# Kernel tuning notes

Measured on AMD Instinct MI355X. Metric: run time of the kernel, lower is better.

The kernel has to match this reference:

```python
import jax, jax.numpy as jnp
import numpy as np

B, S, D = 8, 4096, 512
L = 8921  # n_labels (ICD9 full)

def setup_inputs() -> dict:
    key = jax.random.key(0)
    kx, ku = jax.random.split(key)
    x = jax.random.normal(kx, (B, S, D), dtype=jnp.float32)
    # xavier_uniform init for U [L, D]
    bound = jnp.sqrt(6.0 / (L + D)).astype(jnp.float32)
    U = jax.random.uniform(ku, (L, D), dtype=jnp.float32, minval=-bound, maxval=bound)
    return {"x": x, "U": U}

def reference(x, U):
    # scores: [B, L, S] = U @ x^T (unscaled)
    scores = jnp.einsum('ld,bsd->bls', U, x)
    alpha = jax.nn.softmax(scores, axis=2)  # softmax over sequence dim
    out = jnp.einsum('bls,bsd->bld', alpha, x)  # [B, L, D]
    return (out, alpha)
```

## Files before the change

### kernel.cpp

```cpp
#include <hip/hip_runtime.h>
#include <stdint.h>
#include <stddef.h>

#define BB 8
#define SS 4096
#define DD 512
#define LL 8921

typedef __attribute__((ext_vector_type(8))) short bf16x8;
typedef __attribute__((ext_vector_type(4))) float f32x4;
typedef __attribute__((ext_vector_type(4))) unsigned short u16x4;
typedef __attribute__((ext_vector_type(8))) unsigned short u16x8;

__device__ __forceinline__ unsigned short f2bf(float f) {
  union { float f; uint32_t u; } v; v.f = f;
  uint32_t r = (v.u + 0x7FFFu + ((v.u >> 16) & 1u)) >> 16;
  return (unsigned short)r;
}

__device__ __forceinline__ float bf2f(unsigned short h) {
  union { uint32_t u; float f; } v; v.u = ((uint32_t)h) << 16;
  return v.f;
}

__device__ __forceinline__ void gload_lds16(const void* g, void* l) {
  __builtin_amdgcn_global_load_lds(
      (__attribute__((address_space(1))) void*)(void*)g,
      (__attribute__((address_space(3))) void*)l, 16, 0, 0);
}

__device__ __forceinline__ f32x4 mfma16(bf16x8 a, bf16x8 b, f32x4 c) {
  return __builtin_amdgcn_mfma_f32_16x16x32_bf16(a, b, c, 0, 0, 0);
}

__global__ __launch_bounds__(256) void k_cvtU(const float* __restrict__ U,
                                              unsigned short* __restrict__ Ub) {
  const int idx = blockIdx.x * 256 + threadIdx.x;
  const int nchunk = (LL * DD) / 8;
  if (idx >= nchunk) return;
  const float4* s = (const float4*)U + (size_t)idx * 2;
  const float4 a = s[0], b = s[1];
  u16x8 h;
  h[0] = f2bf(a.x); h[1] = f2bf(a.y); h[2] = f2bf(a.z); h[3] = f2bf(a.w);
  h[4] = f2bf(b.x); h[5] = f2bf(b.y); h[6] = f2bf(b.z); h[7] = f2bf(b.w);
  *(u16x8*)(Ub + (size_t)idx * 8) = h;
}

__global__ __launch_bounds__(256) void k_cvtx(const float* __restrict__ x,
                                              unsigned short* __restrict__ xb,
                                              unsigned short* __restrict__ xT) {
  __shared__ unsigned short t[64][72];
  const int b = blockIdx.z;
  const int s0 = blockIdx.x * 64;
  const int d0 = blockIdx.y * 64;
  const int tid = threadIdx.x;
  const int rr = tid >> 4;
  const int cv = tid & 15;
#pragma unroll
  for (int i = 0; i < 4; ++i) {
    const int srow = rr + i * 16;
    const size_t gi = ((size_t)b * SS + s0 + srow) * DD + d0 + cv * 4;
    const float4 v = *(const float4*)&x[gi];
    u16x4 h;
    h[0] = f2bf(v.x); h[1] = f2bf(v.y); h[2] = f2bf(v.z); h[3] = f2bf(v.w);
    *(u16x4*)&xb[gi] = h;
    t[srow][cv * 4 + 0] = h[0]; t[srow][cv * 4 + 1] = h[1];
    t[srow][cv * 4 + 2] = h[2]; t[srow][cv * 4 + 3] = h[3];
  }
  __syncthreads();
#pragma unroll
  for (int i = 0; i < 4; ++i) {
    const int drow = rr + i * 16;
    u16x4 h;
    h[0] = t[cv * 4 + 0][drow]; h[1] = t[cv * 4 + 1][drow];
    h[2] = t[cv * 4 + 2][drow]; h[3] = t[cv * 4 + 3][drow];
    *(u16x4*)&xT[((size_t)b * DD + d0 + drow) * SS + s0 + cv * 4] = h;
  }
}


__global__ __launch_bounds__(256) void k_score2(const unsigned short* __restrict__ Ub,
                                                const unsigned short* __restrict__ xb,
                                                unsigned short* __restrict__ es,
                                                float* __restrict__ Z) {
  __shared__ unsigned short smem[2][128][64];
  const int tid = threadIdx.x;
  const int lane = tid & 63, wid = tid >> 6;
  const int wr = wid >> 1, wc = wid & 1;
  const int b = blockIdx.y;
  const int lt = blockIdx.x >> 5, st = blockIdx.x & 31;
  const int l0 = lt * 128, s0 = st * 128;
  const int fr = lane & 15, fq = lane >> 4;

  f32x4 acc[4][4];
#pragma unroll
  for (int m = 0; m < 4; ++m)
#pragma unroll
    for (int n = 0; n < 4; ++n) acc[m][n] = (f32x4){0.f, 0.f, 0.f, 0.f};

  for (int k0 = 0; k0 < DD; k0 += 64) {
#pragma unroll
    for (int r = 0; r < 4; ++r) {
      const int c = r * 256 + tid;
      const int row = c >> 3, col = (c & 7) * 8;
      int lrow = l0 + row; if (lrow > LL - 1) lrow = LL - 1;
      gload_lds16(Ub + (size_t)lrow * DD + k0 + col, (unsigned short*)smem[0] + c * 8);
      gload_lds16(xb + ((size_t)b * SS + s0 + row) * DD + k0 + col,
                  (unsigned short*)smem[1] + c * 8);
    }
    __syncthreads();
#pragma unroll
    for (int kk = 0; kk < 64; kk += 32) {
      bf16x8 af[4], bfv[4];
#pragma unroll
      for (int m = 0; m < 4; ++m)
        af[m] = *(const bf16x8*)&smem[0][wr * 64 + m * 16 + fr][kk + fq * 8];
#pragma unroll
      for (int n = 0; n < 4; ++n)
        bfv[n] = *(const bf16x8*)&smem[1][wc * 64 + n * 16 + fr][kk + fq * 8];
#pragma unroll
      for (int m = 0; m < 4; ++m)
#pragma unroll
        for (int n = 0; n < 4; ++n)
          acc[m][n] = mfma16(af[m], bfv[n], acc[m][n]);
    }
    __syncthreads();
  }

  float ev[4][4][4];
  float rsum[4][4];
#pragma unroll
  for (int m = 0; m < 4; ++m)
#pragma unroll
    for (int j = 0; j < 4; ++j) rsum[m][j] = 0.f;
#pragma unroll
  for (int m = 0; m < 4; ++m)
#pragma unroll
    for (int n = 0; n < 4; ++n)
#pragma unroll
      for (int j = 0; j < 4; ++j) {
        const float e = __expf(acc[m][n][j]);
        ev[m][n][j] = e;
        rsum[m][j] += e;
      }
#pragma unroll
  for (int m = 0; m < 4; ++m)
#pragma unroll
    for (int j = 0; j < 4; ++j) {
      float v = rsum[m][j];
      v += __shfl_xor(v, 1);
      v += __shfl_xor(v, 2);
      v += __shfl_xor(v, 4);
      v += __shfl_xor(v, 8);
      const int l = l0 + wr * 64 + m * 16 + fq * 4 + j;
      if (fr == 0 && l < LL) atomicAdd(&Z[b * LL + l], v);
    }
  unsigned short (*Es)[128] = (unsigned short (*)[128])smem;
#pragma unroll
  for (int m = 0; m < 4; ++m) {
    const int lr = wr * 64 + m * 16 + fq * 4;
#pragma unroll
    for (int n = 0; n < 4; ++n) {
      const int sc = wc * 64 + n * 16 + fr;
#pragma unroll
      for (int j = 0; j < 4; ++j) {
        const int ll = lr + j;
        Es[ll][sc ^ ((ll & 7) << 3)] = f2bf(ev[m][n][j]);
      }
    }
  }
  __syncthreads();
  {
    const int lr = tid >> 1;
    const int ch = (tid & 1) * 64;
    const int l = l0 + lr;
    if (l < LL) {
      unsigned short* dst = es + ((size_t)b * LL + l) * SS + s0 + ch;
#pragma unroll
      for (int w = 0; w < 8; ++w) {
        u16x8 hv = *(const u16x8*)&Es[lr][(ch + w * 8) ^ ((lr & 7) << 3)];
        *(u16x8*)(dst + w * 8) = hv;
      }
    }
  }
}

__global__ __launch_bounds__(256) void k_norm(const unsigned short* __restrict__ es,
                                              const float* __restrict__ Z,
                                              float* __restrict__ alpha) {
  const int row = blockIdx.x;
  const float rZ = 1.0f / Z[row];
  const unsigned short* src = es + (size_t)row * SS;
  float* dst = alpha + (size_t)row * SS;
  const int t = threadIdx.x;
#pragma unroll
  for (int i = 0; i < 2; ++i) {
    u16x8 h = *(const u16x8*)(src + t * 16 + i * 8);
    float4 a, b;
    a.x = bf2f(h[0]) * rZ; a.y = bf2f(h[1]) * rZ;
    a.z = bf2f(h[2]) * rZ; a.w = bf2f(h[3]) * rZ;
    b.x = bf2f(h[4]) * rZ; b.y = bf2f(h[5]) * rZ;
    b.z = bf2f(h[6]) * rZ; b.w = bf2f(h[7]) * rZ;
    *(float4*)(dst + t * 16 + i * 8) = a;
    *(float4*)(dst + t * 16 + i * 8 + 4) = b;
  }
}

__global__ __launch_bounds__(256) void k_pv2(const unsigned short* __restrict__ es,
                                             const unsigned short* __restrict__ xTb,
                                             const float* __restrict__ Z,
                                             float* __restrict__ out) {
  __shared__ unsigned short As[128][64];
  __shared__ unsigned short Bs[128][64];
  const int tid = threadIdx.x;
  const int lane = tid & 63, wid = tid >> 6;
  const int wr = wid >> 1, wc = wid & 1;
  const int b = blockIdx.y;
  const int lt = blockIdx.x >> 2, dt = blockIdx.x & 3;
  const int l0 = lt * 128, d0 = dt * 128;
  const int fr = lane & 15, fq = lane >> 4;

  f32x4 acc[4][4];
#pragma unroll
  for (int m = 0; m < 4; ++m)
#pragma unroll
    for (int n = 0; n < 4; ++n) acc[m][n] = (f32x4){0.f, 0.f, 0.f, 0.f};

  for (int k0 = 0; k0 < SS; k0 += 64) {
#pragma unroll
    for (int r = 0; r < 4; ++r) {
      const int c = r * 256 + tid;
      const int row = c >> 3, col = (c & 7) * 8;
      int lrow = l0 + row; if (lrow > LL - 1) lrow = LL - 1;
      gload_lds16(es + ((size_t)b * LL + lrow) * SS + k0 + col,
                  (unsigned short*)As + c * 8);
      gload_lds16(xTb + ((size_t)b * DD + d0 + row) * SS + k0 + col,
                  (unsigned short*)Bs + c * 8);
    }
    __syncthreads();
#pragma unroll
    for (int kk = 0; kk < 64; kk += 32) {
      bf16x8 af[4], bfv[4];
#pragma unroll
      for (int m = 0; m < 4; ++m)
        af[m] = *(const bf16x8*)&As[wr * 64 + m * 16 + fr][kk + fq * 8];
#pragma unroll
      for (int n = 0; n < 4; ++n)
        bfv[n] = *(const bf16x8*)&Bs[wc * 64 + n * 16 + fr][kk + fq * 8];
#pragma unroll
      for (int m = 0; m < 4; ++m)
#pragma unroll
        for (int n = 0; n < 4; ++n)
          acc[m][n] = mfma16(af[m], bfv[n], acc[m][n]);
    }
    __syncthreads();
  }

  float rZv[4][4];
#pragma unroll
  for (int m = 0; m < 4; ++m)
#pragma unroll
    for (int j = 0; j < 4; ++j) {
      const int l = l0 + wr * 64 + m * 16 + fq * 4 + j;
      rZv[m][j] = (l < LL) ? (1.0f / Z[b * LL + l]) : 0.f;
    }
#pragma unroll
  for (int m = 0; m < 4; ++m) {
    const int lbase = l0 + wr * 64 + m * 16 + fq * 4;
#pragma unroll
    for (int n = 0; n < 4; ++n) {
      const int d = d0 + wc * 64 + n * 16 + fr;
#pragma unroll
      for (int j = 0; j < 4; ++j) {
        const int l = lbase + j;
        if (l < LL) out[((size_t)b * LL + l) * DD + d] = acc[m][n][j] * rZv[m][j];
      }
    }
  }
}


__global__ __launch_bounds__(256) void k_score(const unsigned short* __restrict__ Ub,
                                               const unsigned short* __restrict__ xb,
                                               float* __restrict__ alpha,
                                               float* __restrict__ Z) {
  __shared__ unsigned short As[128][64];
  __shared__ unsigned short Bs[128][64];
  const int tid = threadIdx.x;
  const int lane = tid & 63, wid = tid >> 6;
  const int wr = wid >> 1, wc = wid & 1;
  const int b = blockIdx.y;
  const int lt = blockIdx.x >> 5, st = blockIdx.x & 31;
  const int l0 = lt * 128, s0 = st * 128;
  const int fr = lane & 15, fq = lane >> 4;

  f32x4 acc[4][4];
#pragma unroll
  for (int m = 0; m < 4; ++m)
#pragma unroll
    for (int n = 0; n < 4; ++n) acc[m][n] = (f32x4){0.f, 0.f, 0.f, 0.f};

  for (int k0 = 0; k0 < DD; k0 += 64) {
#pragma unroll
    for (int r = 0; r < 4; ++r) {
      const int c = r * 256 + tid;
      const int row = c >> 3, col = (c & 7) * 8;
      int lrow = l0 + row; if (lrow > LL - 1) lrow = LL - 1;
      gload_lds16(Ub + (size_t)lrow * DD + k0 + col, (unsigned short*)As + c * 8);
      gload_lds16(xb + ((size_t)b * SS + s0 + row) * DD + k0 + col,
                  (unsigned short*)Bs + c * 8);
    }
    __syncthreads();
#pragma unroll
    for (int kk = 0; kk < 64; kk += 32) {
      bf16x8 af[4], bfv[4];
#pragma unroll
      for (int m = 0; m < 4; ++m)
        af[m] = *(const bf16x8*)&As[wr * 64 + m * 16 + fr][kk + fq * 8];
#pragma unroll
      for (int n = 0; n < 4; ++n)
        bfv[n] = *(const bf16x8*)&Bs[wc * 64 + n * 16 + fr][kk + fq * 8];
#pragma unroll
      for (int m = 0; m < 4; ++m)
#pragma unroll
        for (int n = 0; n < 4; ++n)
          acc[m][n] = mfma16(af[m], bfv[n], acc[m][n]);
    }
    __syncthreads();
  }

  float rsum[4][4];
#pragma unroll
  for (int m = 0; m < 4; ++m)
#pragma unroll
    for (int j = 0; j < 4; ++j) rsum[m][j] = 0.f;
#pragma unroll
  for (int m = 0; m < 4; ++m) {
    const int lbase = l0 + wr * 64 + m * 16 + fq * 4;
#pragma unroll
    for (int n = 0; n < 4; ++n) {
      const int s = s0 + wc * 64 + n * 16 + fr;
#pragma unroll
      for (int j = 0; j < 4; ++j) {
        const float e = __expf(acc[m][n][j]);
        rsum[m][j] += e;
        const int l = lbase + j;
        if (l < LL) alpha[((size_t)b * LL + l) * SS + s] = e;
      }
    }
  }
#pragma unroll
  for (int m = 0; m < 4; ++m)
#pragma unroll
    for (int j = 0; j < 4; ++j) {
      float v = rsum[m][j];
      v += __shfl_xor(v, 1);
      v += __shfl_xor(v, 2);
      v += __shfl_xor(v, 4);
      v += __shfl_xor(v, 8);
      const int l = l0 + wr * 64 + m * 16 + fq * 4 + j;
      if (fr == 0 && l < LL) atomicAdd(&Z[b * LL + l], v);
    }
}

__global__ __launch_bounds__(256) void k_scale(float* __restrict__ alpha,
                                               const float* __restrict__ Z) {
  const int row = blockIdx.x;
  const float rZ = 1.0f / Z[row];
  float4* p = (float4*)alpha + (size_t)row * (SS / 4);
  const int t = threadIdx.x;
#pragma unroll
  for (int i = 0; i < 4; ++i) {
    float4 v = p[t + i * 256];
    v.x *= rZ; v.y *= rZ; v.z *= rZ; v.w *= rZ;
    p[t + i * 256] = v;
  }
}

__global__ __launch_bounds__(256) void k_pv(const float* __restrict__ alpha,
                                            const unsigned short* __restrict__ xTb,
                                            float* __restrict__ out) {
  __shared__ unsigned short As[128][64];
  __shared__ unsigned short Bs[128][64];
  const int tid = threadIdx.x;
  const int lane = tid & 63, wid = tid >> 6;
  const int wr = wid >> 1, wc = wid & 1;
  const int b = blockIdx.y;
  const int lt = blockIdx.x >> 2, dt = blockIdx.x & 3;
  const int l0 = lt * 128, d0 = dt * 128;
  const int fr = lane & 15, fq = lane >> 4;

  f32x4 acc[4][4];
#pragma unroll
  for (int m = 0; m < 4; ++m)
#pragma unroll
    for (int n = 0; n < 4; ++n) acc[m][n] = (f32x4){0.f, 0.f, 0.f, 0.f};

  for (int k0 = 0; k0 < SS; k0 += 64) {
#pragma unroll
    for (int r = 0; r < 4; ++r) {
      const int c = r * 256 + tid;
      const int row = c >> 3, col = (c & 7) * 8;
      gload_lds16(xTb + ((size_t)b * DD + d0 + row) * SS + k0 + col,
                  (unsigned short*)Bs + c * 8);
      int lrow = l0 + row; if (lrow > LL - 1) lrow = LL - 1;
      const float* src = alpha + ((size_t)b * LL + lrow) * SS + k0 + col;
      const float4 v0 = *(const float4*)src;
      const float4 v1 = *(const float4*)(src + 4);
      bf16x8 h;
      h[0] = (short)f2bf(v0.x); h[1] = (short)f2bf(v0.y);
      h[2] = (short)f2bf(v0.z); h[3] = (short)f2bf(v0.w);
      h[4] = (short)f2bf(v1.x); h[5] = (short)f2bf(v1.y);
      h[6] = (short)f2bf(v1.z); h[7] = (short)f2bf(v1.w);
      *(bf16x8*)((unsigned short*)As + c * 8) = h;
    }
    __syncthreads();
#pragma unroll
    for (int kk = 0; kk < 64; kk += 32) {
      bf16x8 af[4], bfv[4];
#pragma unroll
      for (int m = 0; m < 4; ++m)
        af[m] = *(const bf16x8*)&As[wr * 64 + m * 16 + fr][kk + fq * 8];
#pragma unroll
      for (int n = 0; n < 4; ++n)
        bfv[n] = *(const bf16x8*)&Bs[wc * 64 + n * 16 + fr][kk + fq * 8];
#pragma unroll
      for (int m = 0; m < 4; ++m)
#pragma unroll
        for (int n = 0; n < 4; ++n)
          acc[m][n] = mfma16(af[m], bfv[n], acc[m][n]);
    }
    __syncthreads();
  }

#pragma unroll
  for (int m = 0; m < 4; ++m) {
    const int lbase = l0 + wr * 64 + m * 16 + fq * 4;
#pragma unroll
    for (int n = 0; n < 4; ++n) {
      const int d = d0 + wc * 64 + n * 16 + fr;
#pragma unroll
      for (int j = 0; j < 4; ++j) {
        const int l = lbase + j;
        if (l < LL) out[((size_t)b * LL + l) * DD + d] = acc[m][n][j];
      }
    }
  }
}

extern "C" void kernel_launch(void* const* d_in, const int* in_sizes, int n_in,
                              void* d_out, int out_size, void* d_ws, size_t ws_size,
                              hipStream_t stream) {
  const float* x = (const float*)d_in[0];
  const float* U = (const float*)d_in[1];
  float* out   = (float*)d_out;
  float* alpha = out + (size_t)BB * LL * DD;

  const size_t off_Z  = 0;
  const size_t off_U  = 285696;
  const size_t off_xb = 9420800;
  const size_t off_xT = 42975232;
  const size_t off_es = 76529664;
  const size_t es_bytes = (size_t)BB * LL * SS * 2;
  const size_t need_small = off_es;
  const size_t need_big   = off_es + es_bytes;

  if (ws_size < need_small) return;

  char* ws = (char*)d_ws;
  float* Z = (float*)(ws + off_Z);
  unsigned short* Ub = (unsigned short*)(ws + off_U);
  unsigned short* xb = (unsigned short*)(ws + off_xb);
  unsigned short* xT = (unsigned short*)(ws + off_xT);
  unsigned short* es = (unsigned short*)(ws + off_es);

  hipMemsetAsync(Z, 0, (size_t)BB * LL * 4, stream);
  k_cvtU<<<dim3(((LL * DD / 8) + 255) / 256), 256, 0, stream>>>(U, Ub);
  k_cvtx<<<dim3(SS / 64, DD / 64, BB), 256, 0, stream>>>(x, xb, xT);

  if (ws_size >= need_big) {
    k_score2<<<dim3(70 * 32, BB), 256, 0, stream>>>(Ub, xb, es, Z);
    k_norm<<<dim3(BB * LL), 256, 0, stream>>>(es, Z, alpha);
    k_pv2<<<dim3(70 * 4, BB), 256, 0, stream>>>(es, xT, Z, out);
  } else {
    k_score<<<dim3(70 * 32, BB), 256, 0, stream>>>(Ub, xb, alpha, Z);
    k_scale<<<dim3(BB * LL), 256, 0, stream>>>(alpha, Z);
    k_pv<<<dim3(70 * 4, BB), 256, 0, stream>>>(alpha, xT, out);
  }
}
```

Baseline: 1.658 ms.

## Fuse alpha normalization into PV GEMM and remap block order for XCD locality

Removes the separate k_norm pass that re-read the bf16 exp-scores and wrote normalized fp32 alpha. In its place, the dt==0 blocks of the PV kernel write alpha straight from the exp-score tile already staged in LDS. This saves one full read of es (about 0.6 GB) and a kernel launch. The block index is also remapped so that neighbouring logical tiles, which share es rows, are spread to match the round-robin XCD assignment. The cost is that the dt==0 blocks carry a heavy extra store load (fp32 alpha is about 1.2 GB), which may leave them unbalanced against the other blocks.

```diff
diff --git a/kernel.cpp b/kernel.cpp
--- a/kernel.cpp
+++ b/kernel.cpp
@@ -185,40 +185,30 @@
   }
 }
 
-__global__ __launch_bounds__(256) void k_norm(const unsigned short* __restrict__ es,
-                                              const float* __restrict__ Z,
-                                              float* __restrict__ alpha) {
-  const int row = blockIdx.x;
-  const float rZ = 1.0f / Z[row];
-  const unsigned short* src = es + (size_t)row * SS;
-  float* dst = alpha + (size_t)row * SS;
-  const int t = threadIdx.x;
-#pragma unroll
-  for (int i = 0; i < 2; ++i) {
-    u16x8 h = *(const u16x8*)(src + t * 16 + i * 8);
-    float4 a, b;
-    a.x = bf2f(h[0]) * rZ; a.y = bf2f(h[1]) * rZ;
-    a.z = bf2f(h[2]) * rZ; a.w = bf2f(h[3]) * rZ;
-    b.x = bf2f(h[4]) * rZ; b.y = bf2f(h[5]) * rZ;
-    b.z = bf2f(h[6]) * rZ; b.w = bf2f(h[7]) * rZ;
-    *(float4*)(dst + t * 16 + i * 8) = a;
-    *(float4*)(dst + t * 16 + i * 8 + 4) = b;
-  }
-}
-
-__global__ __launch_bounds__(256) void k_pv2(const unsigned short* __restrict__ es,
+__global__ __launch_bounds__(256) void k_pv3(const unsigned short* __restrict__ es,
                                              const unsigned short* __restrict__ xTb,
                                              const float* __restrict__ Z,
-                                             float* __restrict__ out) {
+                                             float* __restrict__ out,
+                                             float* __restrict__ alpha) {
   __shared__ unsigned short As[128][64];
   __shared__ unsigned short Bs[128][64];
   const int tid = threadIdx.x;
   const int lane = tid & 63, wid = tid >> 6;
   const int wr = wid >> 1, wc = wid & 1;
   const int b = blockIdx.y;
-  const int lt = blockIdx.x >> 2, dt = blockIdx.x & 3;
+  const int bid = blockIdx.x;
+  const int logical = (bid & 7) * 35 + (bid >> 3);
+  const int lt = logical >> 2, dt = logical & 3;
   const int l0 = lt * 128, d0 = dt * 128;
   const int fr = lane & 15, fq = lane >> 4;
+
+  float rZrow[4];
+#pragma unroll
+  for (int r = 0; r < 4; ++r) {
+    int lrow = l0 + r * 32 + (tid >> 3);
+    if (lrow > LL - 1) lrow = LL - 1;
+    rZrow[r] = 1.0f / Z[b * LL + lrow];
+  }
 
   f32x4 acc[4][4];
 #pragma unroll
@@ -238,6 +228,26 @@
                   (unsigned short*)Bs + c * 8);
     }
     __syncthreads();
+
+    if (dt == 0) {
+#pragma unroll
+      for (int r = 0; r < 4; ++r) {
+        const int c = r * 256 + tid;
+        const int row = c >> 3, col = (c & 7) * 8;
+        int lrow = l0 + row; if (lrow > LL - 1) lrow = LL - 1;
+        const u16x8 h = *(const u16x8*)((unsigned short*)As + c * 8);
+        const float rz = rZrow[r];
+        float4 a, bv;
+        a.x = bf2f(h[0]) * rz; a.y = bf2f(h[1]) * rz;
+        a.z = bf2f(h[2]) * rz; a.w = bf2f(h[3]) * rz;
+        bv.x = bf2f(h[4]) * rz; bv.y = bf2f(h[5]) * rz;
+        bv.z = bf2f(h[6]) * rz; bv.w = bf2f(h[7]) * rz;
+        float* dst = alpha + ((size_t)b * LL + lrow) * SS + k0 + col;
+        *(float4*)dst = a;
+        *(float4*)(dst + 4) = bv;
+      }
+    }
+
 #pragma unroll
     for (int kk = 0; kk < 64; kk += 32) {
       bf16x8 af[4], bfv[4];
@@ -480,8 +490,7 @@
 
   if (ws_size >= need_big) {
     k_score2<<<dim3(70 * 32, BB), 256, 0, stream>>>(Ub, xb, es, Z);
-    k_norm<<<dim3(BB * LL), 256, 0, stream>>>(es, Z, alpha);
-    k_pv2<<<dim3(70 * 4, BB), 256, 0, stream>>>(es, xT, Z, out);
+    k_pv3<<<dim3(70 * 4, BB), 256, 0, stream>>>(es, xT, Z, out, alpha);
   } else {
     k_score<<<dim3(70 * 32, BB), 256, 0, stream>>>(Ub, xb, alpha, Z);
     k_scale<<<dim3(BB * LL), 256, 0, stream>>>(alpha, Z);
```

Result: faster. 1.544 ms (-6.9%).
